# Optimization experiments

Measured on AMD Instinct MI355X. Metric: run time of the kernel, lower is better.

Reference implementation:

```python
import jax, jax.numpy as jnp
import numpy as np

DIM = 512
DIM2 = 2 * DIM
HEADS = 8
HEAD_DIM = DIM2 // HEADS
NB = 4                      # BlockDiagonalLinear blocks
BLK = DIM2 // NB
KS = 4                      # causal conv kernel size
EPS = 1e-5


def setup_inputs() -> dict:
    key = jax.random.key(0)
    ks = jax.random.split(key, 32)
    r = lambda i, shape, s=0.02: jax.random.normal(ks[i], shape, dtype=jnp.float32) * s
    inp = {
        "x": jax.random.normal(ks[0], (2, 2048, DIM), dtype=jnp.float32),
        "ln_w": jnp.ones((DIM,), jnp.float32),
        "ln_b": jnp.zeros((DIM,), jnp.float32),
        "mlp1_w": r(1, (DIM, DIM2)), "mlp1_b": jnp.zeros((DIM2,), jnp.float32),
        "mlp2_w": r(2, (DIM, DIM2)), "mlp2_b": jnp.zeros((DIM2,), jnp.float32),
        "conv_w": r(3, (DIM2, DIM2, KS)), "conv_b": jnp.zeros((DIM2,), jnp.float32),
        "bq_w": r(4, (NB, BLK, BLK)), "bk_w": r(5, (NB, BLK, BLK)), "bv_w": r(6, (NB, BLK, BLK)),
        "wq_w": r(7, (DIM2, DIM2)), "wq_b": jnp.zeros((DIM2,), jnp.float32),
        "wk_w": r(8, (DIM2, DIM2)), "wk_b": jnp.zeros((DIM2,), jnp.float32),
        "wv_w": r(9, (DIM2, DIM2)), "wv_b": jnp.zeros((DIM2,), jnp.float32),
        "wi_w": r(10, (DIM2, HEADS)), "wi_b": jnp.zeros((HEADS,), jnp.float32),
        "wf_w": r(11, (DIM2, HEADS)), "wf_b": jnp.zeros((HEADS,), jnp.float32),
        "gn_w": jnp.ones((DIM2,), jnp.float32), "gn_b": jnp.zeros((DIM2,), jnp.float32),
        "skip": jnp.ones((DIM2,), jnp.float32),
        "fin_w": r(12, (DIM2, DIM)), "fin_b": jnp.zeros((DIM,), jnp.float32),
    }
    return inp


def _layernorm(x, w, b):
    mu = jnp.mean(x, -1, keepdims=True)
    var = jnp.var(x, -1, keepdims=True)
    return (x - mu) * jax.lax.rsqrt(var + EPS) * w + b


def _block_linear(x, w):  # x: [b,s,DIM2], w: [NB, BLK, BLK]
    b, s, _ = x.shape
    xg = x.reshape(b, s, NB, BLK)
    return jnp.einsum('bsgi,gio->bsgo', xg, w).reshape(b, s, DIM2)


def _mlstm_cell(q, k, v, wq_w, wq_b, wk_w, wk_b, wv_w, wv_b,
                wi_w, wi_b, wf_w, wf_b, gn_w, gn_b):
    b, s, _ = q.shape
    tau = DIM2 ** 0.5
    itilde = jnp.einsum('bsd,dh->bhs', q, wi_w) + wi_b[None, :, None]   # [b,h,s]
    ftilde = jnp.einsum('bsd,dh->bhs', k, wf_w) + wf_b[None, :, None]   # [b,h,s]
    # cumulative log forget gates; F_act[i,j] = cs[i] - cs[j] on lower triangle
    cs = jnp.cumsum(jax.nn.log_sigmoid(ftilde), axis=-1)                # [b,h,s]
    mask = jnp.tril(jnp.ones((s, s), bool))
    Dtilde = jnp.where(mask,
                       cs[..., :, None] - cs[..., None, :] + itilde[..., None, :],
                       -jnp.inf)                                        # [b,h,s,s]
    max_d = jnp.max(Dtilde, axis=-1, keepdims=True)
    D = jnp.exp(Dtilde - max_d)
    qh = (q @ wq_w + wq_b).reshape(b, s, HEADS, HEAD_DIM).transpose(0, 2, 1, 3)
    kh = (k @ wk_w + wk_b).reshape(b, s, HEADS, HEAD_DIM).transpose(0, 2, 1, 3)
    vh = (v @ wv_w + wv_b).reshape(b, s, HEADS, HEAD_DIM).transpose(0, 2, 1, 3)
    Ctilde = jnp.einsum('bhid,bhjd->bhij', qh, kh) * D / tau
    maxit = jnp.maximum(jnp.abs(Ctilde.sum(-1)), jnp.exp(-max_d[..., 0]))  # [b,h,s]
    H = jnp.einsum('bhij,bhjd->bhid', Ctilde, vh) / (maxit[..., None] + 1e-8)
    H = H.transpose(0, 2, 1, 3)                                          # [b,s,h,hd]
    # GroupNorm(heads, DIM2): per (b,s,head-group) normalization
    mu = jnp.mean(H, -1, keepdims=True)
    var = jnp.var(H, -1, keepdims=True)
    Hn = (H - mu) * jax.lax.rsqrt(var + EPS)
    Hn = Hn * gn_w.reshape(HEADS, HEAD_DIM) + gn_b.reshape(HEADS, HEAD_DIM)
    return Hn.reshape(b, s, DIM2)


def reference(x, ln_w, ln_b, mlp1_w, mlp1_b, mlp2_w, mlp2_b, conv_w, conv_b,
              bq_w, bk_w, bv_w, wq_w, wq_b, wk_w, wk_b, wv_w, wv_b,
              wi_w, wi_b, wf_w, wf_b, gn_w, gn_b, skip, fin_w, fin_b):
    inputs = _layernorm(x, ln_w, ln_b)
    a = inputs @ mlp1_w + mlp1_b                 # [b,s,DIM2]
    bgate = jax.nn.silu(inputs @ mlp2_w + mlp2_b)
    # causal conv1d (left pad KS-1)
    ac = a.transpose(0, 2, 1)                    # [b,DIM2,s]
    qk = jax.lax.conv_general_dilated(ac, conv_w, (1,), [(KS - 1, 0)],
                                      dimension_numbers=('NCH', 'OIH', 'NCH'))
    qk = (qk + conv_b[None, :, None]).transpose(0, 2, 1)
    qk = jax.nn.silu(qk)
    q = _block_linear(qk, bq_w)
    k = _block_linear(qk, bk_w)
    v = _block_linear(a, bv_w)
    out1 = _mlstm_cell(q, k, v, wq_w, wq_b, wk_w, wk_b, wv_w, wv_b,
                       wi_w, wi_b, wf_w, wf_b, gn_w, gn_b)
    out1 = out1 + skip * qk
    out1 = out1 * bgate
    out1 = out1 @ fin_w + fin_b
    return x + out1
```

## Files before the change

kernel.cpp:

```cpp
#include <hip/hip_runtime.h>
#include <hip/hip_bf16.h>
#include <cmath>

typedef __hip_bfloat16 bf16;
typedef __attribute__((ext_vector_type(8))) short short8;
typedef __attribute__((ext_vector_type(4))) float f32x4;

#define SEQ   2048
#define DIMX  512
#define DIM2X 1024
#define NHEADS 8
#define HDIM  128
#define EPSF  1e-5f
#define PADROWS 2051

__device__ __forceinline__ float b2f(bf16 v) { return __bfloat162float(v); }
__device__ __forceinline__ bf16 f2b(float f) { return __float2bfloat16(f); }
__device__ __forceinline__ unsigned short f2bu(float f) { bf16 t = __float2bfloat16(f); return *(unsigned short*)&t; }

__device__ __forceinline__ void gl16(const bf16* g, bf16* l) {
  __builtin_amdgcn_global_load_lds((const __attribute__((address_space(1))) void*)g,
                                   (__attribute__((address_space(3))) void*)l, 16, 0, 0);
}

__global__ void __launch_bounds__(256) k_layernorm(const float* __restrict__ x,
                                                   const float* __restrict__ w,
                                                   const float* __restrict__ b,
                                                   bf16* __restrict__ out) {
  int row  = blockIdx.x * 4 + (threadIdx.x >> 6);
  int lane = threadIdx.x & 63;
  const float* xr = x + (size_t)row * DIMX;
  float v[8]; float s = 0.f, sq = 0.f;
#pragma unroll
  for (int i = 0; i < 8; i++) {
    float f = xr[lane + i * 64];
    v[i] = f; s += f; sq += f * f;
  }
#pragma unroll
  for (int off = 32; off; off >>= 1) { s += __shfl_xor(s, off); sq += __shfl_xor(sq, off); }
  float mu  = s * (1.f / DIMX);
  float var = sq * (1.f / DIMX) - mu * mu;
  float rs  = rsqrtf(var + EPSF);
  bf16* o = out + (size_t)row * DIMX;
#pragma unroll
  for (int i = 0; i < 8; i++) {
    int c = lane + i * 64;
    o[c] = f2b((v[i] - mu) * rs * w[c] + b[c]);
  }
}

__global__ void __launch_bounds__(256) k_castT3(const float* __restrict__ W0,
                                                const float* __restrict__ W1,
                                                const float* __restrict__ W2,
                                                bf16* __restrict__ WT,
                                                int K, int N, int innerZ, int gW, int gT) {
  __shared__ float t[32][33];
  const int z = blockIdx.z;
  const int sel = z / innerZ, zz = z % innerZ;
  const float* W = (sel == 0 ? W0 : sel == 1 ? W1 : W2) + (size_t)zz * gW;
  bf16* T = WT + (size_t)(sel * innerZ + zz) * gT;
  const int k0 = blockIdx.y * 32, n0 = blockIdx.x * 32;
  const int r = threadIdx.x >> 5, c = threadIdx.x & 31;
#pragma unroll
  for (int i = 0; i < 4; i++)
    t[r + i * 8][c] = W[(size_t)(k0 + r + i * 8) * N + n0 + c];
  __syncthreads();
#pragma unroll
  for (int i = 0; i < 4; i++)
    T[(size_t)(n0 + r + i * 8) * K + k0 + c] = f2b(t[c][r + i * 8]);
}

__global__ void __launch_bounds__(256) k_convwT(const float* __restrict__ cw, bf16* __restrict__ wc) {
  int idx = blockIdx.x * 256 + threadIdx.x;
  int o = idx >> 12, z = idx & 4095, kk = z >> 10, i = z & 1023;
  wc[idx] = f2b(cw[(size_t)o * 4096 + i * 4 + kk]);
}

__global__ void __launch_bounds__(256) k_zeropad(bf16* __restrict__ p) {
  int idx = blockIdx.x * 256 + threadIdx.x;
  int b = idx / 3072, off = idx % 3072;
  p[(size_t)b * PADROWS * DIM2X + off] = f2b(0.f);
}

__device__ __forceinline__ void mgemm_body(const bf16* A, int lda, const bf16* WT,
                                           const float* bias, void* Cv, const float* xres,
                                           int ldc, int K, int ACT, int STORE, int APAD,
                                           size_t coff) {
  __shared__ __align__(16) bf16 smA[4][128 * 32];
  __shared__ __align__(16) bf16 smB[4][64 * 32];
  const int tid  = threadIdx.x;
  const int lane = tid & 63;
  const int w = tid >> 6, wy = w >> 1, wx = w & 1;
  const int col = lane & 15, quad = lane >> 4;
  const int bm = blockIdx.y * 128, bn = blockIdx.x * 64;

  const int r4 = tid >> 2, c8 = (tid & 3) * 8;
  int ra0 = bm + r4, ra1 = bm + 64 + r4;
  if (APAD) { ra0 += (ra0 >> 11) * 3 + 3; ra1 += (ra1 >> 11) * 3 + 3; }
  const bf16* gA0 = A + (size_t)ra0 * lda + c8;
  const bf16* gA1 = A + (size_t)ra1 * lda + c8;
  const bf16* gB0 = WT + (size_t)(bn + r4) * K + c8;

  f32x4 acc[4][2];
#pragma unroll
  for (int a = 0; a < 4; a++)
#pragma unroll
    for (int b = 0; b < 2; b++) acc[a][b] = (f32x4){0.f, 0.f, 0.f, 0.f};

  const int laoff = (wy * 64) * 32, lboff = (wx * 32) * 32;
  const int lsa = r4 * 32 + c8;
  const int nsteps = K >> 5;

#define GSTAGE(buf, k0s)                                                       \
  do {                                                                         \
    gl16(gA0 + (k0s), &smA[buf][lsa]);                                         \
    gl16(gA1 + (k0s), &smA[buf][64 * 32 + lsa]);                               \
    gl16(gB0 + (k0s), &smB[buf][lsa]);                                         \
  } while (0)

  GSTAGE(0, 0);
  if (nsteps > 1) GSTAGE(1, 32);
  for (int s = 0; s < nsteps; ++s) {
    if (s + 2 < nsteps) GSTAGE((s + 2) & 3, (s + 2) * 32);
    if (s + 2 < nsteps)      asm volatile("s_waitcnt vmcnt(6)" ::: "memory");
    else if (s + 1 < nsteps) asm volatile("s_waitcnt vmcnt(3)" ::: "memory");
    else                     asm volatile("s_waitcnt vmcnt(0)" ::: "memory");
    __builtin_amdgcn_s_barrier();
    asm volatile("" ::: "memory");
    const bf16* bA = smA[s & 3];
    const bf16* bB = smB[s & 3];
    short8 af[4], bfr[2];
#pragma unroll
    for (int mt = 0; mt < 4; mt++)
      af[mt] = *(const short8*)&bA[laoff + (mt * 16 + col) * 32 + quad * 8];
#pragma unroll
    for (int nt = 0; nt < 2; nt++)
      bfr[nt] = *(const short8*)&bB[lboff + (nt * 16 + col) * 32 + quad * 8];
#pragma unroll
    for (int mt = 0; mt < 4; mt++)
#pragma unroll
      for (int nt = 0; nt < 2; nt++)
        acc[mt][nt] = __builtin_amdgcn_mfma_f32_16x16x32_bf16(af[mt], bfr[nt], acc[mt][nt], 0, 0, 0);
  }
#undef GSTAGE

#pragma unroll
  for (int mt = 0; mt < 4; mt++) {
#pragma unroll
    for (int nt = 0; nt < 2; nt++) {
      const int n = bn + wx * 32 + nt * 16 + col;
      const int mrow0 = bm + wy * 64 + mt * 16 + quad * 4;
      float bs = bias ? bias[n] : 0.f;
      if (STORE == 1) {
        bf16* C = (bf16*)Cv + coff;
        ushort4 pk;
        pk.x = f2bu(acc[mt][nt][0] + bs); pk.y = f2bu(acc[mt][nt][1] + bs);
        pk.z = f2bu(acc[mt][nt][2] + bs); pk.w = f2bu(acc[mt][nt][3] + bs);
        *(ushort4*)(C + (size_t)n * 4096 + mrow0) = pk;
      } else if (STORE == 2) {
        float* O = (float*)Cv + coff;
#pragma unroll
        for (int r = 0; r < 4; r++) {
          size_t gi = (size_t)(mrow0 + r) * ldc + n;
          O[gi] = acc[mt][nt][r] + bs + xres[gi];
        }
      } else if (STORE == 3) {
        bf16* C = (bf16*)Cv;
        const int pr = (mrow0 >> 11) * 3 + 3;
#pragma unroll
        for (int r = 0; r < 4; r++)
          C[(size_t)(mrow0 + pr + r) * ldc + n] = f2b(acc[mt][nt][r] + bs);
      } else {
        bf16* C = (bf16*)Cv + coff;
#pragma unroll
        for (int r = 0; r < 4; r++) {
          float v = acc[mt][nt][r] + bs;
          if (ACT == 1) v = v / (1.f + expf(-v));
          C[(size_t)(mrow0 + r) * ldc + n] = f2b(v);
        }
      }
    }
  }
}

template <int ACT, int STORE, int APAD>
__global__ void __launch_bounds__(256) k_mgemm(const bf16* __restrict__ A, int lda,
                                               const bf16* __restrict__ WT,
                                               const float* __restrict__ bias,
                                               void* __restrict__ Cv,
                                               const float* __restrict__ xres,
                                               int ldc, int K,
                                               int gA, int gW, int gC) {
  const int g = blockIdx.z;
  mgemm_body(A + (size_t)g * gA, lda, WT + (size_t)g * gW, bias, Cv, xres,
             ldc, K, ACT, STORE, APAD, (size_t)g * gC);
}

__global__ void __launch_bounds__(256) k_mgemmB(const bf16* A0, const bf16* A1, const bf16* A2,
                                                const bf16* W0, const bf16* W1, const bf16* W2,
                                                const float* b0, const float* b1, const float* b2,
                                                void* C0, void* C1, void* C2,
                                                int lda, int ldc, int K, int zPer,
                                                int gA, int gW, int gC,
                                                int actm, int storem, int apadm) {
  const int z = blockIdx.z;
  const int sel = z / zPer, zz = z % zPer;
  const bf16* A = (sel == 0 ? A0 : sel == 1 ? A1 : A2) + (size_t)zz * gA;
  const bf16* W = (sel == 0 ? W0 : sel == 1 ? W1 : W2) + (size_t)zz * gW;
  const float* bias = sel == 0 ? b0 : sel == 1 ? b1 : b2;
  void* Cv = sel == 0 ? C0 : sel == 1 ? C1 : C2;
  mgemm_body(A, lda, W, bias, Cv, nullptr, ldc, K,
             (actm >> sel) & 1, (storem >> (4 * sel)) & 15, (apadm >> sel) & 1,
             (size_t)zz * gC);
}

__global__ void __launch_bounds__(256) k_gates(const bf16* __restrict__ q, const bf16* __restrict__ kk,
                                               const float* __restrict__ wi, const float* __restrict__ wib,
                                               const float* __restrict__ wf, const float* __restrict__ wfb,
                                               float* __restrict__ it, float* __restrict__ ft) {
  int gid  = blockIdx.x * 4 + (threadIdx.x >> 6);
  int lane = threadIdx.x & 63;
  int which = gid >> 12;
  int m = gid & 4095;
  const bf16* row = (which ? kk : q) + (size_t)m * DIM2X;
  const float* w = which ? wf : wi;
  float s[8] = {0, 0, 0, 0, 0, 0, 0, 0};
  for (int d = lane; d < DIM2X; d += 64) {
    float xv = b2f(row[d]);
    const float4* wp = (const float4*)(w + d * 8);
    float4 w0 = wp[0], w1 = wp[1];
    s[0] += xv * w0.x; s[1] += xv * w0.y; s[2] += xv * w0.z; s[3] += xv * w0.w;
    s[4] += xv * w1.x; s[5] += xv * w1.y; s[6] += xv * w1.z; s[7] += xv * w1.w;
  }
#pragma unroll
  for (int off = 32; off; off >>= 1) {
#pragma unroll
    for (int h = 0; h < 8; h++) s[h] += __shfl_xor(s[h], off);
  }
  if (lane == 0) {
    int b_ = m >> 11, tt = m & 2047;
    const float* wb = which ? wfb : wib;
    float* dst = which ? ft : it;
#pragma unroll
    for (int h = 0; h < 8; h++)
      dst[((size_t)(b_ * NHEADS + h)) * SEQ + tt] = s[h] + wb[h];
  }
}

__global__ void __launch_bounds__(256) k_scan(const float* __restrict__ it, const float* __restrict__ ft,
                                              float* __restrict__ cs, float* __restrict__ md) {
  const int bh = blockIdx.x;
  const int t  = threadIdx.x;
  const float* fr = ft + (size_t)bh * SEQ;
  const float* ir = it + (size_t)bh * SEQ;
  float* csr = cs + (size_t)bh * SEQ;
  float* mdr = md + (size_t)bh * SEQ;
  __shared__ float tmp[256];
  float loc[8]; float run = 0.f;
#pragma unroll
  for (int j = 0; j < 8; j++) {
    float xv = fr[t * 8 + j];
    float ls = fminf(xv, 0.f) - log1pf(expf(-fabsf(xv)));
    run += ls; loc[j] = run;
  }
  tmp[t] = run;
  __syncthreads();
  for (int off = 1; off < 256; off <<= 1) {
    float add = (t >= off) ? tmp[t - off] : 0.f;
    __syncthreads();
    tmp[t] += add;
    __syncthreads();
  }
  float exc = (t == 0) ? 0.f : tmp[t - 1];
  float csv[8];
#pragma unroll
  for (int j = 0; j < 8; j++) { csv[j] = loc[j] + exc; csr[t * 8 + j] = csv[j]; }
  __syncthreads();
  float rmax = -INFINITY; float gm[8];
#pragma unroll
  for (int j = 0; j < 8; j++) {
    float gv = ir[t * 8 + j] - csv[j];
    rmax = fmaxf(rmax, gv); gm[j] = rmax;
  }
  tmp[t] = rmax;
  __syncthreads();
  for (int off = 1; off < 256; off <<= 1) {
    float other = (t >= off) ? tmp[t - off] : -INFINITY;
    __syncthreads();
    tmp[t] = fmaxf(tmp[t], other);
    __syncthreads();
  }
  float emax = (t == 0) ? -INFINITY : tmp[t - 1];
#pragma unroll
  for (int j = 0; j < 8; j++) mdr[t * 8 + j] = csv[j] + fmaxf(gm[j], emax);
}

__global__ void __launch_bounds__(256) k_attn_mfma(const bf16* __restrict__ qh,
                                                   const bf16* __restrict__ kh,
                                                   const bf16* __restrict__ vt,
                                                   const float* __restrict__ cs,
                                                   const float* __restrict__ md,
                                                   const float* __restrict__ itl,
                                                   bf16* __restrict__ Hout) {
  const int bh = blockIdx.y, b_ = bh >> 3, h = bh & 7;
  const int bx = blockIdx.x;
  const int tile = ((blockIdx.y >> 3) & 1) ? bx : 31 - bx;
  const int i0 = tile * 64;
  const int tid = threadIdx.x;
  const int w = tid >> 6;
  const int lane = tid & 63;
  const int col = lane & 15, quad = lane >> 4;
  const int i0w = i0 + w * 16;
  const int iwmax = i0w + 15;
  const float L2E = 1.44269504f;

  __shared__ __align__(16) bf16 smK[4 * 4096];
  __shared__ __align__(16) bf16 smV[4 * 4096];
  __shared__ __align__(16) bf16 Sc[4][16][40];

  const size_t baseQK = ((size_t)b_ * SEQ) * DIM2X + (size_t)h * HDIM;
  const size_t vtb = (size_t)(h * HDIM) * 4096 + (size_t)b_ * SEQ;
  const float* csp = cs + (size_t)bh * SEQ;
  const float* mdp = md + (size_t)bh * SEQ;
  const float* itp = itl + (size_t)bh * SEQ;

  short8 qf[4];
#pragma unroll
  for (int kc = 0; kc < 4; kc++)
    qf[kc] = *(const short8*)(qh + baseQK + (size_t)(i0w + col) * DIM2X + kc * 32 + quad * 8);

  float cs_i[4], md_i[4];
#pragma unroll
  for (int r = 0; r < 4; r++) {
    int i = i0w + quad * 4 + r;
    cs_i[r] = csp[i] * L2E; md_i[r] = mdp[i] * L2E;
  }

  f32x4 accpv[8];
#pragma unroll
  for (int nb = 0; nb < 8; nb++) accpv[nb] = (f32x4){0.f, 0.f, 0.f, 0.f};
  float rs[4] = {0.f, 0.f, 0.f, 0.f};

  const int kj = tid >> 4, kq = tid & 15;
  const bf16* gKs = kh + baseQK + (size_t)kj * DIM2X + ((kq ^ (kj & 7)) * 8);
  const int vn = tid >> 2, vq = tid & 3;
  const bf16* gVs = vt + vtb + (size_t)vn * 4096 + ((vq ^ ((vn >> 1) & 3)) * 8);

  const int trips = 2 * tile + 2;

#define STAGE(buf, j0s)                                                        \
  do {                                                                         \
    bf16* dK = &smK[(buf) * 4096 + tid * 8];                                   \
    gl16(gKs + (size_t)(j0s) * DIM2X, dK);                                     \
    gl16(gKs + (size_t)((j0s) + 16) * DIM2X, dK + 2048);                       \
    bf16* dV = &smV[(buf) * 4096 + tid * 8];                                   \
    gl16(gVs + (j0s), dV);                                                     \
    gl16(gVs + (j0s) + (size_t)64 * 4096, dV + 2048);                          \
  } while (0)

  STAGE(0, 0);
  STAGE(1, 32);
  for (int t = 0; t < trips; ++t) {
    const int cur = t & 3;
    const int j0p = t * 32;
    if (t + 2 < trips) STAGE((t + 2) & 3, j0p + 64);
    if (t + 2 < trips)      asm volatile("s_waitcnt vmcnt(8)" ::: "memory");
    else if (t + 1 < trips) asm volatile("s_waitcnt vmcnt(4)" ::: "memory");
    else                    asm volatile("s_waitcnt vmcnt(0)" ::: "memory");
    __builtin_amdgcn_s_barrier();
    asm volatile("" ::: "memory");
    if (j0p <= iwmax) {
      float g0 = (itp[j0p + col] - csp[j0p + col]) * L2E;
      float g1 = (itp[j0p + 16 + col] - csp[j0p + 16 + col]) * L2E;
      const bool jt1 = (j0p + 16 <= iwmax);
#pragma unroll
      for (int jt = 0; jt < 2; jt++) {
        const int j0 = j0p + jt * 16;
        float sv[4] = {0.f, 0.f, 0.f, 0.f};
        if (jt == 0 || jt1) {
          const int jj = jt * 16 + col;
          f32x4 aq = (f32x4){0.f, 0.f, 0.f, 0.f};
#pragma unroll
          for (int kc = 0; kc < 4; kc++) {
            short8 bk = *(const short8*)&smK[cur * 4096 + jj * 128 + ((((kc << 2) | quad) ^ (jj & 7)) << 3)];
            aq = __builtin_amdgcn_mfma_f32_16x16x32_bf16(qf[kc], bk, aq, 0, 0, 0);
          }
          const int j = j0 + col;
          const float gj = jt ? g1 : g0;
#pragma unroll
          for (int r = 0; r < 4; r++) {
            const int i = i0w + quad * 4 + r;
            float s = (j <= i) ? exp2f(cs_i[r] + gj - md_i[r] - 5.f) * aq[r] : 0.f;
            sv[r] = s; rs[r] += s;
          }
        }
#pragma unroll
        for (int r = 0; r < 4; r++) Sc[w][quad * 4 + r][jt * 16 + col] = f2b(sv[r]);
      }
      asm volatile("s_waitcnt lgkmcnt(0)" ::: "memory");
      __builtin_amdgcn_sched_barrier(0);
      short8 af = *(const short8*)(&Sc[w][col][quad * 8]);
#pragma unroll
      for (int nb = 0; nb < 8; nb++) {
        const int rn = nb * 16 + col;
        short8 bv = *(const short8*)&smV[cur * 4096 + rn * 32 + ((quad ^ ((rn >> 1) & 3)) << 3)];
        accpv[nb] = __builtin_amdgcn_mfma_f32_16x16x32_bf16(af, bv, accpv[nb], 0, 0, 0);
      }
    }
  }
#undef STAGE

#pragma unroll
  for (int r = 0; r < 4; r++) {
    float v = rs[r];
    v += __shfl_xor(v, 1); v += __shfl_xor(v, 2);
    v += __shfl_xor(v, 4); v += __shfl_xor(v, 8);
    rs[r] = v;
  }
  float inv[4];
#pragma unroll
  for (int r = 0; r < 4; r++) {
    float maxit = fmaxf(fabsf(rs[r]), exp2f(fminf(-md_i[r], 43.f)));
    inv[r] = 1.f / (maxit + 1e-8f);
  }
#pragma unroll
  for (int nb = 0; nb < 8; nb++)
#pragma unroll
    for (int r = 0; r < 4; r++)
      Hout[baseQK + (size_t)(i0w + quad * 4 + r) * DIM2X + nb * 16 + col] = f2b(accpv[nb][r] * inv[r]);
}

__global__ void __launch_bounds__(256) k_gnorm(const bf16* __restrict__ H, const bf16* __restrict__ qk,
                                               const bf16* __restrict__ bg,
                                               const float* __restrict__ gw, const float* __restrict__ gb,
                                               const float* __restrict__ skip, bf16* __restrict__ pre) {
  int gid  = blockIdx.x * 4 + (threadIdx.x >> 6);
  int lane = threadIdx.x & 63;
  int m = gid >> 3, h = gid & 7;
  const bf16* Hr = H + (size_t)m * DIM2X + (size_t)h * HDIM;
  float v0 = b2f(Hr[lane]), v1 = b2f(Hr[lane + 64]);
  float s = v0 + v1, sq = v0 * v0 + v1 * v1;
#pragma unroll
  for (int off = 32; off; off >>= 1) { s += __shfl_xor(s, off); sq += __shfl_xor(sq, off); }
  float mu  = s * (1.f / 128.f);
  float var = sq * (1.f / 128.f) - mu * mu;
  float rs  = rsqrtf(var + EPSF);
#pragma unroll
  for (int e = 0; e < 2; e++) {
    int c = lane + e * 64;
    int col = h * HDIM + c;
    float v = e ? v1 : v0;
    float hn = (v - mu) * rs * gw[col] + gb[col];
    size_t gidx = (size_t)m * DIM2X + col;
    pre[gidx] = f2b((hn + skip[col] * b2f(qk[gidx])) * b2f(bg[gidx]));
  }
}

extern "C" void kernel_launch(void* const* d_in, const int* in_sizes, int n_in,
                              void* d_out, int out_size, void* d_ws, size_t ws_size,
                              hipStream_t stream) {
  const float* x     = (const float*)d_in[0];
  const float* ln_w  = (const float*)d_in[1];
  const float* ln_b  = (const float*)d_in[2];
  const float* mlp1w = (const float*)d_in[3];
  const float* mlp1b = (const float*)d_in[4];
  const float* mlp2w = (const float*)d_in[5];
  const float* mlp2b = (const float*)d_in[6];
  const float* convw = (const float*)d_in[7];
  const float* convb = (const float*)d_in[8];
  const float* bqw   = (const float*)d_in[9];
  const float* bkw   = (const float*)d_in[10];
  const float* bvw   = (const float*)d_in[11];
  const float* wqw   = (const float*)d_in[12];
  const float* wqb   = (const float*)d_in[13];
  const float* wkw   = (const float*)d_in[14];
  const float* wkb   = (const float*)d_in[15];
  const float* wvw   = (const float*)d_in[16];
  const float* wvb   = (const float*)d_in[17];
  const float* wiw   = (const float*)d_in[18];
  const float* wib   = (const float*)d_in[19];
  const float* wfw   = (const float*)d_in[20];
  const float* wfb   = (const float*)d_in[21];
  const float* gnw   = (const float*)d_in[22];
  const float* gnb   = (const float*)d_in[23];
  const float* skip  = (const float*)d_in[24];
  const float* finw  = (const float*)d_in[25];
  const float* finb  = (const float*)d_in[26];
  float* out = (float*)d_out;

  float* GA  = (float*)d_ws;
  float* ITb = GA;
  float* FTb = GA + 32768;
  float* CSb = GA + 65536;
  float* MDb = GA + 98304;
  const size_t SLOT = 4u * 1024u * 1024u;
  bf16* S0 = (bf16*)((char*)d_ws + (1 << 20));
  bf16* S1 = S0 + SLOT;
  bf16* S2 = S1 + SLOT;
  bf16* S3 = S2 + SLOT;
  bf16* S4 = S3 + SLOT;
  bf16* S5 = S4 + SLOT;
  bf16* S6 = S5 + SLOT;
  bf16 *LN = S0, *BG = S2, *QKb = S3, *Qb = S4, *Kb = S5, *Vb = S6;
  bf16 *QH = S0, *KH = S1, *VT = S4, *Hb = S5, *PRE = S6;
  bf16* WTb   = S6 + SLOT;
  bf16* mlp1T = WTb;
  bf16* mlp2T = WTb + 524288;
  bf16* convT = WTb + 1048576;
  bf16* bqT   = WTb + 5242880;
  bf16* bkT   = bqT + 262144;
  bf16* bvT   = bkT + 262144;
  bf16* wqT   = bvT + 262144;
  bf16* wkT   = wqT + 1048576;
  bf16* wvT   = wkT + 1048576;
  bf16* finT  = wvT + 1048576;
  bf16* APD   = finT + 524288;

  k_castT3<<<dim3(32, 16, 2), 256, 0, stream>>>(mlp1w, mlp2w, mlp2w, mlp1T, DIMX, DIM2X, 1, 0, 524288);
  k_castT3<<<dim3(32, 32, 3), 256, 0, stream>>>(wqw, wkw, wvw, wqT, DIM2X, DIM2X, 1, 0, 1048576);
  k_castT3<<<dim3(8, 8, 12), 256, 0, stream>>>(bqw, bkw, bvw, bqT, 256, 256, 4, 65536, 65536);
  k_castT3<<<dim3(16, 32, 1), 256, 0, stream>>>(finw, finw, finw, finT, DIM2X, DIMX, 1, 0, 524288);
  k_convwT<<<16384, 256, 0, stream>>>(convw, convT);
  k_zeropad<<<24, 256, 0, stream>>>(APD);

  k_layernorm<<<1024, 256, 0, stream>>>(x, ln_w, ln_b, LN);
  k_mgemmB<<<dim3(16, 32, 2), 256, 0, stream>>>(LN, LN, LN, mlp1T, mlp2T, mlp2T,
                                                mlp1b, mlp2b, mlp2b, APD, BG, BG,
                                                DIMX, DIM2X, DIMX, 1, 0, 0, 0,
                                                 0b10,  3 | (0 << 4),  0);
  k_mgemm<1, 0, 0><<<dim3(16, 16, 2), 256, 0, stream>>>(APD, DIM2X, convT, convb, QKb, nullptr,
                                                        DIM2X, 4096, PADROWS * DIM2X, 0, SEQ * DIM2X);
  k_mgemmB<<<dim3(4, 32, 12), 256, 0, stream>>>(QKb, QKb, APD, bqT, bkT, bvT,
                                                nullptr, nullptr, nullptr, Qb, Kb, Vb,
                                                DIM2X, DIM2X, 256, 4, 256, 65536, 256,
                                                 0,  0,  0b100);
  k_gates<<<2048, 256, 0, stream>>>(Qb, Kb, wiw, wib, wfw, wfb, ITb, FTb);
  k_scan<<<16, 256, 0, stream>>>(ITb, FTb, CSb, MDb);
  k_mgemmB<<<dim3(16, 32, 3), 256, 0, stream>>>(Qb, Kb, Vb, wqT, wkT, wvT,
                                                wqb, wkb, wvb, QH, KH, VT,
                                                DIM2X, DIM2X, DIM2X, 1, 0, 0, 0,
                                                 0,  0 | (0 << 4) | (1 << 8),  0);
  k_attn_mfma<<<dim3(32, 16), 256, 0, stream>>>(QH, KH, VT, CSb, MDb, ITb, Hb);
  k_gnorm<<<8192, 256, 0, stream>>>(Hb, QKb, BG, gnw, gnb, skip, PRE);
  k_mgemm<0, 2, 0><<<dim3(8, 32), 256, 0, stream>>>(PRE, DIM2X, finT, finb, out, x, DIMX, DIM2X, 0, 0, 0);
}
```

Baseline: 471.7 us.

## Pair causal attention tiles per block and remap GEMM blocks across XCDs

The causal attention kernel now gives each block two query tiles (tile p and 31-p), so every block does the same total work and the grid shrinks from 512 to 256 blocks. This removes the load imbalance from triangular causal work but halves parallelism. Separately, GEMM blocks are remapped so consecutive logical tiles land on the same XCD, aiming to improve L2 reuse of shared A/W tiles. The remap assumes the total block count is divisible by 8 and that hardware dispatches blocks to XCDs round-robin.

```diff
diff --git a/kernel.cpp b/kernel.cpp
--- a/kernel.cpp
+++ b/kernel.cpp
@@ -85,14 +85,13 @@
 __device__ __forceinline__ void mgemm_body(const bf16* A, int lda, const bf16* WT,
                                            const float* bias, void* Cv, const float* xres,
                                            int ldc, int K, int ACT, int STORE, int APAD,
-                                           size_t coff) {
+                                           size_t coff, int bm, int bn) {
   __shared__ __align__(16) bf16 smA[4][128 * 32];
   __shared__ __align__(16) bf16 smB[4][64 * 32];
   const int tid  = threadIdx.x;
   const int lane = tid & 63;
   const int w = tid >> 6, wy = w >> 1, wx = w & 1;
   const int col = lane & 15, quad = lane >> 4;
-  const int bm = blockIdx.y * 128, bn = blockIdx.x * 64;
 
   const int r4 = tid >> 2, c8 = (tid & 3) * 8;
   int ra0 = bm + r4, ra1 = bm + 64 + r4;
@@ -183,6 +182,13 @@
   }
 }
 
+__device__ __forceinline__ int xcd_work_id() {
+  const int nx = gridDim.x, ny = gridDim.y;
+  const int d = blockIdx.x + nx * (blockIdx.y + ny * blockIdx.z);
+  const int q = (nx * ny * (int)gridDim.z) >> 3;
+  return (d & 7) * q + (d >> 3);
+}
+
 template <int ACT, int STORE, int APAD>
 __global__ void __launch_bounds__(256) k_mgemm(const bf16* __restrict__ A, int lda,
                                                const bf16* __restrict__ WT,
@@ -191,9 +197,12 @@
                                                const float* __restrict__ xres,
                                                int ldc, int K,
                                                int gA, int gW, int gC) {
-  const int g = blockIdx.z;
+  const int wk = xcd_work_id();
+  const int nx = gridDim.x, ny = gridDim.y;
+  const int wx = wk % nx, rest = wk / nx;
+  const int wy = rest % ny, g = rest / ny;
   mgemm_body(A + (size_t)g * gA, lda, WT + (size_t)g * gW, bias, Cv, xres,
-             ldc, K, ACT, STORE, APAD, (size_t)g * gC);
+             ldc, K, ACT, STORE, APAD, (size_t)g * gC, wy * 128, wx * 64);
 }
 
 __global__ void __launch_bounds__(256) k_mgemmB(const bf16* A0, const bf16* A1, const bf16* A2,
@@ -203,7 +212,10 @@
                                                 int lda, int ldc, int K, int zPer,
                                                 int gA, int gW, int gC,
                                                 int actm, int storem, int apadm) {
-  const int z = blockIdx.z;
+  const int wk = xcd_work_id();
+  const int nx = gridDim.x, ny = gridDim.y;
+  const int wx = wk % nx, rest = wk / nx;
+  const int wy = rest % ny, z = rest / ny;
   const int sel = z / zPer, zz = z % zPer;
   const bf16* A = (sel == 0 ? A0 : sel == 1 ? A1 : A2) + (size_t)zz * gA;
   const bf16* W = (sel == 0 ? W0 : sel == 1 ? W1 : W2) + (size_t)zz * gW;
@@ -211,7 +223,7 @@
   void* Cv = sel == 0 ? C0 : sel == 1 ? C1 : C2;
   mgemm_body(A, lda, W, bias, Cv, nullptr, ldc, K,
              (actm >> sel) & 1, (storem >> (4 * sel)) & 15, (apadm >> sel) & 1,
-             (size_t)zz * gC);
+             (size_t)zz * gC, wy * 128, wx * 64);
 }
 
 __global__ void __launch_bounds__(256) k_gates(const bf16* __restrict__ q, const bf16* __restrict__ kk,
@@ -303,15 +315,11 @@
                                                    const float* __restrict__ itl,
                                                    bf16* __restrict__ Hout) {
   const int bh = blockIdx.y, b_ = bh >> 3, h = bh & 7;
-  const int bx = blockIdx.x;
-  const int tile = ((blockIdx.y >> 3) & 1) ? bx : 31 - bx;
-  const int i0 = tile * 64;
+  const int pr = blockIdx.x;
   const int tid = threadIdx.x;
   const int w = tid >> 6;
   const int lane = tid & 63;
   const int col = lane & 15, quad = lane >> 4;
-  const int i0w = i0 + w * 16;
-  const int iwmax = i0w + 15;
   const float L2E = 1.44269504f;
 
   __shared__ __align__(16) bf16 smK[4 * 4096];
@@ -324,29 +332,10 @@
   const float* mdp = md + (size_t)bh * SEQ;
   const float* itp = itl + (size_t)bh * SEQ;
 
-  short8 qf[4];
-#pragma unroll
-  for (int kc = 0; kc < 4; kc++)
-    qf[kc] = *(const short8*)(qh + baseQK + (size_t)(i0w + col) * DIM2X + kc * 32 + quad * 8);
-
-  float cs_i[4], md_i[4];
-#pragma unroll
-  for (int r = 0; r < 4; r++) {
-    int i = i0w + quad * 4 + r;
-    cs_i[r] = csp[i] * L2E; md_i[r] = mdp[i] * L2E;
-  }
-
-  f32x4 accpv[8];
-#pragma unroll
-  for (int nb = 0; nb < 8; nb++) accpv[nb] = (f32x4){0.f, 0.f, 0.f, 0.f};
-  float rs[4] = {0.f, 0.f, 0.f, 0.f};
-
   const int kj = tid >> 4, kq = tid & 15;
   const bf16* gKs = kh + baseQK + (size_t)kj * DIM2X + ((kq ^ (kj & 7)) * 8);
   const int vn = tid >> 2, vq = tid & 3;
   const bf16* gVs = vt + vtb + (size_t)vn * 4096 + ((vq ^ ((vn >> 1) & 3)) * 8);
-
-  const int trips = 2 * tile + 2;
 
 #define STAGE(buf, j0s)                                                        \
   do {                                                                         \
@@ -358,76 +347,102 @@
     gl16(gVs + (j0s) + (size_t)64 * 4096, dV + 2048);                          \
   } while (0)
 
-  STAGE(0, 0);
-  STAGE(1, 32);
-  for (int t = 0; t < trips; ++t) {
-    const int cur = t & 3;
-    const int j0p = t * 32;
-    if (t + 2 < trips) STAGE((t + 2) & 3, j0p + 64);
-    if (t + 2 < trips)      asm volatile("s_waitcnt vmcnt(8)" ::: "memory");
-    else if (t + 1 < trips) asm volatile("s_waitcnt vmcnt(4)" ::: "memory");
-    else                    asm volatile("s_waitcnt vmcnt(0)" ::: "memory");
-    __builtin_amdgcn_s_barrier();
-    asm volatile("" ::: "memory");
-    if (j0p <= iwmax) {
-      float g0 = (itp[j0p + col] - csp[j0p + col]) * L2E;
-      float g1 = (itp[j0p + 16 + col] - csp[j0p + 16 + col]) * L2E;
-      const bool jt1 = (j0p + 16 <= iwmax);
-#pragma unroll
-      for (int jt = 0; jt < 2; jt++) {
-        const int j0 = j0p + jt * 16;
-        float sv[4] = {0.f, 0.f, 0.f, 0.f};
-        if (jt == 0 || jt1) {
-          const int jj = jt * 16 + col;
-          f32x4 aq = (f32x4){0.f, 0.f, 0.f, 0.f};
-#pragma unroll
-          for (int kc = 0; kc < 4; kc++) {
-            short8 bk = *(const short8*)&smK[cur * 4096 + jj * 128 + ((((kc << 2) | quad) ^ (jj & 7)) << 3)];
-            aq = __builtin_amdgcn_mfma_f32_16x16x32_bf16(qf[kc], bk, aq, 0, 0, 0);
+  for (int ph = 0; ph < 2; ++ph) {
+    const int tile = ph ? (31 - pr) : pr;
+    const int i0 = tile * 64;
+    const int i0w = i0 + w * 16;
+    const int iwmax = i0w + 15;
+
+    short8 qf[4];
+#pragma unroll
+    for (int kc = 0; kc < 4; kc++)
+      qf[kc] = *(const short8*)(qh + baseQK + (size_t)(i0w + col) * DIM2X + kc * 32 + quad * 8);
+
+    float cs_i[4], md_i[4];
+#pragma unroll
+    for (int r = 0; r < 4; r++) {
+      int i = i0w + quad * 4 + r;
+      cs_i[r] = csp[i] * L2E; md_i[r] = mdp[i] * L2E;
+    }
+
+    f32x4 accpv[8];
+#pragma unroll
+    for (int nb = 0; nb < 8; nb++) accpv[nb] = (f32x4){0.f, 0.f, 0.f, 0.f};
+    float rs[4] = {0.f, 0.f, 0.f, 0.f};
+
+    const int trips = 2 * tile + 2;
+    STAGE(0, 0);
+    STAGE(1, 32);
+    for (int t = 0; t < trips; ++t) {
+      const int cur = t & 3;
+      const int j0p = t * 32;
+      if (t + 2 < trips) STAGE((t + 2) & 3, j0p + 64);
+      if (t + 2 < trips)      asm volatile("s_waitcnt vmcnt(8)" ::: "memory");
+      else if (t + 1 < trips) asm volatile("s_waitcnt vmcnt(4)" ::: "memory");
+      else                    asm volatile("s_waitcnt vmcnt(0)" ::: "memory");
+      __builtin_amdgcn_s_barrier();
+      asm volatile("" ::: "memory");
+      if (j0p <= iwmax) {
+        float g0 = (itp[j0p + col] - csp[j0p + col]) * L2E;
+        float g1 = (itp[j0p + 16 + col] - csp[j0p + 16 + col]) * L2E;
+        const bool jt1 = (j0p + 16 <= iwmax);
+#pragma unroll
+        for (int jt = 0; jt < 2; jt++) {
+          const int j0 = j0p + jt * 16;
+          float sv[4] = {0.f, 0.f, 0.f, 0.f};
+          if (jt == 0 || jt1) {
+            const int jj = jt * 16 + col;
+            f32x4 aq = (f32x4){0.f, 0.f, 0.f, 0.f};
+#pragma unroll
+            for (int kc = 0; kc < 4; kc++) {
+              short8 bk = *(const short8*)&smK[cur * 4096 + jj * 128 + ((((kc << 2) | quad) ^ (jj & 7)) << 3)];
+              aq = __builtin_amdgcn_mfma_f32_16x16x32_bf16(qf[kc], bk, aq, 0, 0, 0);
+            }
+            const int j = j0 + col;
+            const float gj = jt ? g1 : g0;
+#pragma unroll
+            for (int r = 0; r < 4; r++) {
+              const int i = i0w + quad * 4 + r;
+              float s = (j <= i) ? exp2f(cs_i[r] + gj - md_i[r] - 5.f) * aq[r] : 0.f;
+              sv[r] = s; rs[r] += s;
+            }
           }
-          const int j = j0 + col;
-          const float gj = jt ? g1 : g0;
-#pragma unroll
-          for (int r = 0; r < 4; r++) {
-            const int i = i0w + quad * 4 + r;
-            float s = (j <= i) ? exp2f(cs_i[r] + gj - md_i[r] - 5.f) * aq[r] : 0.f;
-            sv[r] = s; rs[r] += s;
-          }
+#pragma unroll
+          for (int r = 0; r < 4; r++) Sc[w][quad * 4 + r][jt * 16 + col] = f2b(sv[r]);
         }
-#pragma unroll
-        for (int r = 0; r < 4; r++) Sc[w][quad * 4 + r][jt * 16 + col] = f2b(sv[r]);
-      }
-      asm volatile("s_waitcnt lgkmcnt(0)" ::: "memory");
-      __builtin_amdgcn_sched_barrier(0);
-      short8 af = *(const short8*)(&Sc[w][col][quad * 8]);
-#pragma unroll
-      for (int nb = 0; nb < 8; nb++) {
-        const int rn = nb * 16 + col;
-        short8 bv = *(const short8*)&smV[cur * 4096 + rn * 32 + ((quad ^ ((rn >> 1) & 3)) << 3)];
-        accpv[nb] = __builtin_amdgcn_mfma_f32_16x16x32_bf16(af, bv, accpv[nb], 0, 0, 0);
+        asm volatile("s_waitcnt lgkmcnt(0)" ::: "memory");
+        __builtin_amdgcn_sched_barrier(0);
+        short8 af = *(const short8*)(&Sc[w][col][quad * 8]);
+#pragma unroll
+        for (int nb = 0; nb < 8; nb++) {
+          const int rn = nb * 16 + col;
+          short8 bv = *(const short8*)&smV[cur * 4096 + rn * 32 + ((quad ^ ((rn >> 1) & 3)) << 3)];
+          accpv[nb] = __builtin_amdgcn_mfma_f32_16x16x32_bf16(af, bv, accpv[nb], 0, 0, 0);
+        }
       }
     }
+    __syncthreads();
+
+#pragma unroll
+    for (int r = 0; r < 4; r++) {
+      float v = rs[r];
+      v += __shfl_xor(v, 1); v += __shfl_xor(v, 2);
+      v += __shfl_xor(v, 4); v += __shfl_xor(v, 8);
+      rs[r] = v;
+    }
+    float inv[4];
+#pragma unroll
+    for (int r = 0; r < 4; r++) {
+      float maxit = fmaxf(fabsf(rs[r]), exp2f(fminf(-md_i[r], 43.f)));
+      inv[r] = 1.f / (maxit + 1e-8f);
+    }
+#pragma unroll
+    for (int nb = 0; nb < 8; nb++)
+#pragma unroll
+      for (int r = 0; r < 4; r++)
+        Hout[baseQK + (size_t)(i0w + quad * 4 + r) * DIM2X + nb * 16 + col] = f2b(accpv[nb][r] * inv[r]);
   }
 #undef STAGE
-
-#pragma unroll
-  for (int r = 0; r < 4; r++) {
-    float v = rs[r];
-    v += __shfl_xor(v, 1); v += __shfl_xor(v, 2);
-    v += __shfl_xor(v, 4); v += __shfl_xor(v, 8);
-    rs[r] = v;
-  }
-  float inv[4];
-#pragma unroll
-  for (int r = 0; r < 4; r++) {
-    float maxit = fmaxf(fabsf(rs[r]), exp2f(fminf(-md_i[r], 43.f)));
-    inv[r] = 1.f / (maxit + 1e-8f);
-  }
-#pragma unroll
-  for (int nb = 0; nb < 8; nb++)
-#pragma unroll
-    for (int r = 0; r < 4; r++)
-      Hout[baseQK + (size_t)(i0w + quad * 4 + r) * DIM2X + nb * 16 + col] = f2b(accpv[nb][r] * inv[r]);
 }
 
 __global__ void __launch_bounds__(256) k_gnorm(const bf16* __restrict__ H, const bf16* __restrict__ qk,
@@ -540,7 +555,7 @@
                                                 wqb, wkb, wvb, QH, KH, VT,
                                                 DIM2X, DIM2X, DIM2X, 1, 0, 0, 0,
                                                  0,  0 | (0 << 4) | (1 << 8),  0);
-  k_attn_mfma<<<dim3(32, 16), 256, 0, stream>>>(QH, KH, VT, CSb, MDb, ITb, Hb);
+  k_attn_mfma<<<dim3(16, 16), 256, 0, stream>>>(QH, KH, VT, CSb, MDb, ITb, Hb);
   k_gnorm<<<8192, 256, 0, stream>>>(Hb, QKb, BG, gnw, gnb, skip, PRE);
   k_mgemm<0, 2, 0><<<dim3(8, 32), 256, 0, stream>>>(PRE, DIM2X, finT, finb, out, x, DIMX, DIM2X, 0, 0, 0);
 }
```

After: 460.5 us. 2.4% less time.
